# Kernel tuning notes

Measured on AMD Instinct MI355X. Metric: run time of the kernel, lower is better.

The kernel has to match this reference:

```python
import jax, jax.numpy as jnp
import numpy as np

N_HEADS = 8

def setup_inputs() -> dict:
    key = jax.random.key(0)
    ks = jax.random.split(key, 5)
    C = 256
    x = jax.random.normal(ks[0], (4, C, 48, 48), dtype=jnp.float32)
    w_qkv = jax.random.normal(ks[1], (3 * C, C), dtype=jnp.float32) * (C ** -0.5)
    b_qkv = jax.random.normal(ks[2], (3 * C,), dtype=jnp.float32) * 0.02
    w_proj = jax.random.normal(ks[3], (C, C), dtype=jnp.float32) * (C ** -0.5)
    b_proj = jax.random.normal(ks[4], (C,), dtype=jnp.float32) * 0.02
    return {"x": x, "w_qkv": w_qkv, "b_qkv": b_qkv, "w_proj": w_proj, "b_proj": b_proj}


def reference(x, w_qkv, b_qkv, w_proj, b_proj):
    B, C, H, W = x.shape
    h = N_HEADS
    dh = C // h
    N = H * W
    # flatten spatial dims to tokens: [B, N, C]
    xf = x.reshape(B, C, N).transpose(0, 2, 1)
    # fused qkv projection (torch Linear: y = x @ W.T + b)
    qkv = xf @ w_qkv.T + b_qkv                      # [B, N, 3C]
    qkv = qkv.reshape(B, N, 3, h, dh).transpose(2, 0, 3, 1, 4)  # [3, B, h, N, dh]
    q, k, v = qkv[0], qkv[1], qkv[2]
    scale = dh ** -0.5
    attn = jax.nn.softmax(jnp.einsum('bhnd,bhmd->bhnm', q, k) * scale, axis=-1)
    out = jnp.einsum('bhnm,bhmd->bhnd', attn, v)    # [B, h, N, dh]
    out = out.transpose(0, 2, 1, 3).reshape(B, N, C)
    out = out @ w_proj.T + b_proj                   # [B, N, C]
    return out.transpose(0, 2, 1).reshape(B, C, H, W)
```

## Files before the change

### kernel.cpp

```cpp
#include <hip/hip_runtime.h>
#include <hip/hip_bf16.h>

#define B_    4
#define C_    256
#define NTOK  2304
#define NH    8
#define DH    32

typedef short bf16x8 __attribute__((ext_vector_type(8)));
typedef short bf16x4 __attribute__((ext_vector_type(4)));
typedef float f32x4  __attribute__((ext_vector_type(4)));

__device__ __forceinline__ short f2bf(float f) {
    __hip_bfloat16 h = __float2bfloat16(f);
    return *reinterpret_cast<short*>(&h);
}

__global__ __launch_bounds__(256) void prep_kernel(
    const float* __restrict__ x, const float* __restrict__ wq,
    const float* __restrict__ wp,
    short* __restrict__ xt, short* __restrict__ wqb, short* __restrict__ wpb)
{
    const int blk = blockIdx.x;
    const int t   = threadIdx.x;
    if (blk < 576) {
        const int b  = blk / 144;
        const int rem = blk % 144;
        const int n0 = (rem / 4) * 64;
        const int c0 = (rem % 4) * 64;
        __shared__ float tile[64][65];
        const float* xb = x + ((size_t)b * C_ + c0) * NTOK + n0;
        const int n = t & 63, cc = t >> 6;
        #pragma unroll
        for (int r = 0; r < 16; ++r)
            tile[cc + r * 4][n] = xb[(size_t)(cc + r * 4) * NTOK + n];
        __syncthreads();
        const int nr = t >> 2, cb = (t & 3) * 16;
        short* dst = xt + ((size_t)b * NTOK + n0 + nr) * C_ + c0 + cb;
        bf16x8 v0, v1;
        #pragma unroll
        for (int u = 0; u < 8; ++u) v0[u] = f2bf(tile[cb + u][nr]);
        #pragma unroll
        for (int u = 0; u < 8; ++u) v1[u] = f2bf(tile[cb + 8 + u][nr]);
        *(bf16x8*)dst = v0;
        *(bf16x8*)(dst + 8) = v1;
    } else {
        const int id = (blk - 576) * 256 + t;
        const int base = id * 16;
        #pragma unroll
        for (int u = 0; u < 4; ++u) {
            const int off = base + u * 4;
            float4 v; short* d;
            if (off < 196608) { v = *(const float4*)(wq + off); d = wqb + off; }
            else { v = *(const float4*)(wp + (off - 196608)); d = wpb + (off - 196608); }
            d[0] = f2bf(v.x); d[1] = f2bf(v.y); d[2] = f2bf(v.z); d[3] = f2bf(v.w);
        }
    }
}

__global__ __launch_bounds__(256) void qkv_mfma(
    const short* __restrict__ xt,
    const short* __restrict__ wqb,
    const float* __restrict__ bias,
    short* __restrict__ qb, short* __restrict__ kb, short* __restrict__ vt)
{
    const int wid  = blockIdx.x * 4 + (threadIdx.x >> 6);
    const int lane = threadIdx.x & 63;
    const int quad = lane >> 4, l16 = lane & 15;
    const int b   = wid / 432;
    const int rem = wid % 432;
    const int mt = rem / 12, nt = rem % 12;
    const int m0 = mt * 64, j0 = nt * 64;

    const short* abase = xt + ((size_t)b * NTOK + m0 + l16) * C_ + quad * 8;
    const short* bbase = wqb + (size_t)(j0 + l16) * C_ + quad * 8;

    f32x4 acc[4][4] = {};
    for (int k0 = 0; k0 < C_; k0 += 32) {
        bf16x8 af[4], bfr[4];
        #pragma unroll
        for (int i = 0; i < 4; ++i)
            af[i] = *(const bf16x8*)(abase + (size_t)i * 16 * C_ + k0);
        #pragma unroll
        for (int j = 0; j < 4; ++j)
            bfr[j] = *(const bf16x8*)(bbase + (size_t)j * 16 * C_ + k0);
        #pragma unroll
        for (int i = 0; i < 4; ++i)
            #pragma unroll
            for (int j = 0; j < 4; ++j)
                acc[i][j] = __builtin_amdgcn_mfma_f32_16x16x32_bf16(af[i], bfr[j], acc[i][j], 0, 0, 0);
    }

    const int three = j0 >> 8;
    const float scale = 0.17677669529663687f;
    #pragma unroll
    for (int j = 0; j < 4; ++j) {
        const int jg   = j0 + j * 16 + l16;
        const int head = (jg >> 5) & 7;
        const int d    = jg & 31;
        const float bv = bias[jg];
        const size_t bhbase = (size_t)(b * NH + head) * NTOK;
        #pragma unroll
        for (int i = 0; i < 4; ++i) {
            if (three == 2) {
                bf16x4 pv;
                #pragma unroll
                for (int r = 0; r < 4; ++r) pv[r] = f2bf(acc[i][j][r] + bv);
                *(bf16x4*)(vt + ((size_t)(b * NH + head) * DH + d) * NTOK
                              + m0 + i * 16 + quad * 4) = pv;
            } else {
                short* dst = (three == 0) ? qb : kb;
                const float sc = (three == 0) ? scale : 1.0f;
                #pragma unroll
                for (int r = 0; r < 4; ++r) {
                    const int n = m0 + i * 16 + quad * 4 + r;
                    dst[(bhbase + n) * DH + d] = f2bf((acc[i][j][r] + bv) * sc);
                }
            }
        }
    }
}

__global__ __launch_bounds__(256) void attn_kernel(
    const short* __restrict__ qg,
    const short* __restrict__ kg,
    const short* __restrict__ vg,
    short* __restrict__ ob)
{
    const int bh   = blockIdx.y;
    const int q0   = blockIdx.x * 64;
    const int t    = threadIdx.x;
    const int wave = t >> 6;
    const int lane = t & 63;
    const int quad = lane >> 4;
    const int l16  = lane & 15;

    __shared__ short Ks[64][40];
    __shared__ short Vt[32][72];
    __shared__ short Ps[4][16][68];

    const short* kbase = kg + (size_t)bh * NTOK * DH;
    const short* vbase = vg + (size_t)bh * DH * NTOK;

    const short* qptr = qg + ((size_t)bh * NTOK + q0 + wave * 16 + l16) * DH + quad * 8;
    const bf16x8 qf = *(const bf16x8*)qptr;

    f32x4 Oc0 = {0.f, 0.f, 0.f, 0.f};
    f32x4 Oc1 = {0.f, 0.f, 0.f, 0.f};
    float lpart[4] = {0.f, 0.f, 0.f, 0.f};

    for (int kt = 0; kt < NTOK; kt += 64) {
        {
            const int kr = t >> 2, ksg = t & 3;
            *(bf16x8*)&Ks[kr][ksg * 8] =
                *(const bf16x8*)(kbase + (size_t)(kt + kr) * DH + ksg * 8);
            const int vr = t >> 3, vsg = t & 7;
            *(bf16x8*)&Vt[vr][vsg * 8] =
                *(const bf16x8*)(vbase + (size_t)vr * NTOK + kt + vsg * 8);
        }
        __syncthreads();

        f32x4 S[4];
        #pragma unroll
        for (int jt = 0; jt < 4; ++jt) {
            const bf16x8 kf = *(const bf16x8*)&Ks[jt * 16 + l16][quad * 8];
            f32x4 z = {0.f, 0.f, 0.f, 0.f};
            S[jt] = __builtin_amdgcn_mfma_f32_16x16x32_bf16(qf, kf, z, 0, 0, 0);
        }

        #pragma unroll
        for (int jt = 0; jt < 4; ++jt) {
            #pragma unroll
            for (int r = 0; r < 4; ++r) {
                const float p = __expf(S[jt][r]);
                lpart[r] += p;
                Ps[wave][quad * 4 + r][jt * 16 + l16] = f2bf(p);
            }
        }

        #pragma unroll
        for (int jc = 0; jc < 2; ++jc) {
            const bf16x4 p0 = *(const bf16x4*)&Ps[wave][l16][jc * 32 + quad * 8];
            const bf16x4 p1 = *(const bf16x4*)&Ps[wave][l16][jc * 32 + quad * 8 + 4];
            bf16x8 af;
            af[0] = p0[0]; af[1] = p0[1]; af[2] = p0[2]; af[3] = p0[3];
            af[4] = p1[0]; af[5] = p1[1]; af[6] = p1[2]; af[7] = p1[3];
            const bf16x8 b0 = *(const bf16x8*)&Vt[l16][jc * 32 + quad * 8];
            const bf16x8 b1 = *(const bf16x8*)&Vt[16 + l16][jc * 32 + quad * 8];
            Oc0 = __builtin_amdgcn_mfma_f32_16x16x32_bf16(af, b0, Oc0, 0, 0, 0);
            Oc1 = __builtin_amdgcn_mfma_f32_16x16x32_bf16(af, b1, Oc1, 0, 0, 0);
        }
        __syncthreads();
    }

    #pragma unroll
    for (int off = 1; off < 16; off <<= 1) {
        #pragma unroll
        for (int r = 0; r < 4; ++r)
            lpart[r] += __shfl_xor(lpart[r], off, 64);
    }
    short* obase = ob + ((size_t)bh * NTOK + q0 + wave * 16 + quad * 4) * DH + l16;
    #pragma unroll
    for (int r = 0; r < 4; ++r) {
        const float inv = 1.f / lpart[r];
        obase[(size_t)r * DH]      = f2bf(Oc0[r] * inv);
        obase[(size_t)r * DH + 16] = f2bf(Oc1[r] * inv);
    }
}

__global__ __launch_bounds__(256) void proj_mfma(
    const short* __restrict__ ab,
    const short* __restrict__ wpb,
    const float* __restrict__ bias,
    float* __restrict__ out)
{
    const int wid  = blockIdx.x * 4 + (threadIdx.x >> 6);
    const int lane = threadIdx.x & 63;
    const int quad = lane >> 4, l16 = lane & 15;
    const int b   = wid / 144;
    const int rem = wid % 144;
    const int mt = rem / 4, nt = rem % 4;
    const int m0 = mt * 64, c0 = nt * 64;

    const short* bbase = wpb + (size_t)(c0 + l16) * C_ + quad * 8;

    f32x4 acc[4][4] = {};
    for (int kt = 0; kt < 8; ++kt) {
        const short* abase = ab + ((size_t)(b * NH + kt) * NTOK + m0 + l16) * DH + quad * 8;
        bf16x8 af[4], bfr[4];
        #pragma unroll
        for (int i = 0; i < 4; ++i)
            af[i] = *(const bf16x8*)(abase + (size_t)i * 16 * DH);
        #pragma unroll
        for (int j = 0; j < 4; ++j)
            bfr[j] = *(const bf16x8*)(bbase + (size_t)j * 16 * C_ + kt * 32);
        #pragma unroll
        for (int i = 0; i < 4; ++i)
            #pragma unroll
            for (int j = 0; j < 4; ++j)
                acc[i][j] = __builtin_amdgcn_mfma_f32_16x16x32_bf16(af[i], bfr[j], acc[i][j], 0, 0, 0);
    }

    #pragma unroll
    for (int j = 0; j < 4; ++j) {
        const int c    = c0 + j * 16 + l16;
        const float bv = bias[c];
        #pragma unroll
        for (int i = 0; i < 4; ++i) {
            float4 st = {acc[i][j][0] + bv, acc[i][j][1] + bv,
                         acc[i][j][2] + bv, acc[i][j][3] + bv};
            *(float4*)(out + ((size_t)b * C_ + c) * NTOK + m0 + i * 16 + quad * 4) = st;
        }
    }
}

extern "C" void kernel_launch(void* const* d_in, const int* in_sizes, int n_in,
                              void* d_out, int out_size, void* d_ws, size_t ws_size,
                              hipStream_t stream) {
    const float* x      = (const float*)d_in[0];
    const float* w_qkv  = (const float*)d_in[1];
    const float* b_qkv  = (const float*)d_in[2];
    const float* w_proj = (const float*)d_in[3];
    const float* b_proj = (const float*)d_in[4];
    float* out = (float*)d_out;

    const size_t SZ = (size_t)B_ * NH * NTOK * DH;
    short* xt  = (short*)d_ws;
    short* wqb = xt + SZ;
    short* wpb = wqb + 196608;
    short* qb  = wpb + 65536;
    short* kb  = qb + SZ;
    short* vt  = kb + SZ;
    short* abf = vt + SZ;

    prep_kernel<<<640, 256, 0, stream>>>(x, w_qkv, w_proj, xt, wqb, wpb);
    qkv_mfma<<<432, 256, 0, stream>>>(xt, wqb, b_qkv, qb, kb, vt);
    attn_kernel<<<dim3(36, 32), 256, 0, stream>>>(qb, kb, vt, abf);
    proj_mfma<<<144, 256, 0, stream>>>(abf, wpb, b_proj, out);
}
```

Measured before the change: 167.1 us.

## Halve GEMM tiles, stage epilogues through LDS, widen attention key tile, use exp2

The QKV and projection GEMMs now use 32-row tiles per wave and launch twice as many blocks. Their epilogues are staged through per-wave shared memory so that global stores become coalesced 16-byte vectors instead of scattered 2-byte or 4-byte writes. The attention loop processes 128 keys per iteration, which halves the number of barriers, and it computes exp2 with the log2(e) factor folded into the Q scale. A manual round-to-nearest-even bf16 conversion replaces the library call. The costs are more LDS use per block and fewer MFMA operations per loaded fragment in the GEMMs.

```diff
diff --git a/kernel.cpp b/kernel.cpp
--- a/kernel.cpp
+++ b/kernel.cpp
@@ -11,9 +11,20 @@
 typedef short bf16x4 __attribute__((ext_vector_type(4)));
 typedef float f32x4  __attribute__((ext_vector_type(4)));
 
-__device__ __forceinline__ short f2bf(float f) {
-    __hip_bfloat16 h = __float2bfloat16(f);
-    return *reinterpret_cast<short*>(&h);
+__device__ __forceinline__ short rne_bf16(float f) {
+    union { float f; unsigned u; } v; v.f = f;
+    const unsigned r = v.u + 0x7fffu + ((v.u >> 16) & 1u);
+    return (short)(r >> 16);
+}
+__device__ __forceinline__ unsigned pack2_bf16(float a, float b) {
+    return (unsigned)(unsigned short)rne_bf16(a) | ((unsigned)(unsigned short)rne_bf16(b) << 16);
+}
+__device__ __forceinline__ float fast_exp2(float x) {
+#if __has_builtin(__builtin_amdgcn_exp2f)
+    return __builtin_amdgcn_exp2f(x);
+#else
+    return exp2f(x);
+#endif
 }
 
 __global__ __launch_bounds__(256) void prep_kernel(
@@ -39,9 +50,9 @@
         short* dst = xt + ((size_t)b * NTOK + n0 + nr) * C_ + c0 + cb;
         bf16x8 v0, v1;
         #pragma unroll
-        for (int u = 0; u < 8; ++u) v0[u] = f2bf(tile[cb + u][nr]);
-        #pragma unroll
-        for (int u = 0; u < 8; ++u) v1[u] = f2bf(tile[cb + 8 + u][nr]);
+        for (int u = 0; u < 8; ++u) v0[u] = rne_bf16(tile[cb + u][nr]);
+        #pragma unroll
+        for (int u = 0; u < 8; ++u) v1[u] = rne_bf16(tile[cb + 8 + u][nr]);
         *(bf16x8*)dst = v0;
         *(bf16x8*)(dst + 8) = v1;
     } else {
@@ -53,7 +64,8 @@
             float4 v; short* d;
             if (off < 196608) { v = *(const float4*)(wq + off); d = wqb + off; }
             else { v = *(const float4*)(wp + (off - 196608)); d = wpb + (off - 196608); }
-            d[0] = f2bf(v.x); d[1] = f2bf(v.y); d[2] = f2bf(v.z); d[3] = f2bf(v.w);
+            d[0] = rne_bf16(v.x); d[1] = rne_bf16(v.y);
+            d[2] = rne_bf16(v.z); d[3] = rne_bf16(v.w);
         }
     }
 }
@@ -64,59 +76,79 @@
     const float* __restrict__ bias,
     short* __restrict__ qb, short* __restrict__ kb, short* __restrict__ vt)
 {
-    const int wid  = blockIdx.x * 4 + (threadIdx.x >> 6);
+    __shared__ short Es[4][2560];
+    const int wave = threadIdx.x >> 6;
     const int lane = threadIdx.x & 63;
     const int quad = lane >> 4, l16 = lane & 15;
-    const int b   = wid / 432;
-    const int rem = wid % 432;
+    const int wid  = blockIdx.x * 4 + wave;
+    const int b    = wid / 864;
+    const int rem  = wid % 864;
     const int mt = rem / 12, nt = rem % 12;
-    const int m0 = mt * 64, j0 = nt * 64;
+    const int m0 = mt * 32, j0 = nt * 64;
 
     const short* abase = xt + ((size_t)b * NTOK + m0 + l16) * C_ + quad * 8;
     const short* bbase = wqb + (size_t)(j0 + l16) * C_ + quad * 8;
 
-    f32x4 acc[4][4] = {};
+    f32x4 acc[2][4] = {};
     for (int k0 = 0; k0 < C_; k0 += 32) {
-        bf16x8 af[4], bfr[4];
-        #pragma unroll
-        for (int i = 0; i < 4; ++i)
+        bf16x8 af[2], bfr[4];
+        #pragma unroll
+        for (int i = 0; i < 2; ++i)
             af[i] = *(const bf16x8*)(abase + (size_t)i * 16 * C_ + k0);
         #pragma unroll
         for (int j = 0; j < 4; ++j)
             bfr[j] = *(const bf16x8*)(bbase + (size_t)j * 16 * C_ + k0);
         #pragma unroll
-        for (int i = 0; i < 4; ++i)
+        for (int i = 0; i < 2; ++i)
             #pragma unroll
             for (int j = 0; j < 4; ++j)
                 acc[i][j] = __builtin_amdgcn_mfma_f32_16x16x32_bf16(af[i], bfr[j], acc[i][j], 0, 0, 0);
     }
 
+    short* Ew = Es[wave];
     const int three = j0 >> 8;
-    const float scale = 0.17677669529663687f;
-    #pragma unroll
-    for (int j = 0; j < 4; ++j) {
-        const int jg   = j0 + j * 16 + l16;
-        const int head = (jg >> 5) & 7;
-        const int d    = jg & 31;
-        const float bv = bias[jg];
-        const size_t bhbase = (size_t)(b * NH + head) * NTOK;
-        #pragma unroll
-        for (int i = 0; i < 4; ++i) {
-            if (three == 2) {
-                bf16x4 pv;
-                #pragma unroll
-                for (int r = 0; r < 4; ++r) pv[r] = f2bf(acc[i][j][r] + bv);
-                *(bf16x4*)(vt + ((size_t)(b * NH + head) * DH + d) * NTOK
-                              + m0 + i * 16 + quad * 4) = pv;
-            } else {
-                short* dst = (three == 0) ? qb : kb;
-                const float sc = (three == 0) ? scale : 1.0f;
+    if (three < 2) {
+        const float sc = (three == 0) ? 0.25503486f : 1.0f;
+        #pragma unroll
+        for (int j = 0; j < 4; ++j) {
+            const float bv = bias[j0 + j * 16 + l16];
+            #pragma unroll
+            for (int i = 0; i < 2; ++i)
                 #pragma unroll
                 for (int r = 0; r < 4; ++r) {
-                    const int n = m0 + i * 16 + quad * 4 + r;
-                    dst[(bhbase + n) * DH + d] = f2bf((acc[i][j][r] + bv) * sc);
+                    const int n_l = i * 16 + quad * 4 + r;
+                    Ew[n_l * 72 + j * 16 + l16] = rne_bf16((acc[i][j][r] + bv) * sc);
                 }
+        }
+        const int n_l = lane & 31, hh = lane >> 5;
+        const int head = ((j0 + hh * 32) >> 5) & 7;
+        short* dst = ((three == 0) ? qb : kb)
+                   + ((size_t)(b * NH + head) * NTOK + m0 + n_l) * DH;
+        #pragma unroll
+        for (int s = 0; s < 4; ++s)
+            *(bf16x8*)(dst + s * 8) = *(const bf16x8*)&Ew[n_l * 72 + hh * 32 + s * 8];
+    } else {
+        #pragma unroll
+        for (int j = 0; j < 4; ++j) {
+            const float bv = bias[j0 + j * 16 + l16];
+            const int j_l = j * 16 + l16;
+            #pragma unroll
+            for (int i = 0; i < 2; ++i) {
+                const int nb = i * 16 + quad * 4;
+                *(unsigned*)&Ew[j_l * 40 + nb] =
+                    pack2_bf16(acc[i][j][0] + bv, acc[i][j][1] + bv);
+                *(unsigned*)&Ew[j_l * 40 + nb + 2] =
+                    pack2_bf16(acc[i][j][2] + bv, acc[i][j][3] + bv);
             }
+        }
+        #pragma unroll
+        for (int p = 0; p < 4; ++p) {
+            const int j_r = p * 16 + (lane >> 2);
+            const int seg = (lane & 3) * 8;
+            const int head = ((j0 + j_r) >> 5) & 7;
+            const int d    = j_r & 31;
+            *(bf16x8*)(vt + ((size_t)(b * NH + head) * DH + d) * NTOK + m0 + seg) =
+                *(const bf16x8*)&Ew[j_r * 40 + seg];
         }
     }
 }
@@ -135,9 +167,9 @@
     const int quad = lane >> 4;
     const int l16  = lane & 15;
 
-    __shared__ short Ks[64][40];
-    __shared__ short Vt[32][72];
-    __shared__ short Ps[4][16][68];
+    __shared__ short Ks[128][40];
+    __shared__ short Vt[32][168];
+    __shared__ short Ps[4][16][140];
 
     const short* kbase = kg + (size_t)bh * NTOK * DH;
     const short* vbase = vg + (size_t)bh * DH * NTOK;
@@ -149,37 +181,39 @@
     f32x4 Oc1 = {0.f, 0.f, 0.f, 0.f};
     float lpart[4] = {0.f, 0.f, 0.f, 0.f};
 
-    for (int kt = 0; kt < NTOK; kt += 64) {
-        {
-            const int kr = t >> 2, ksg = t & 3;
-            *(bf16x8*)&Ks[kr][ksg * 8] =
-                *(const bf16x8*)(kbase + (size_t)(kt + kr) * DH + ksg * 8);
-            const int vr = t >> 3, vsg = t & 7;
-            *(bf16x8*)&Vt[vr][vsg * 8] =
-                *(const bf16x8*)(vbase + (size_t)vr * NTOK + kt + vsg * 8);
+    for (int kt = 0; kt < NTOK; kt += 128) {
+        #pragma unroll
+        for (int u = 0; u < 2; ++u) {
+            const int chunk = u * 256 + t;
+            const int krow = chunk >> 2, kseg = chunk & 3;
+            *(bf16x8*)&Ks[krow][kseg * 8] =
+                *(const bf16x8*)(kbase + (size_t)(kt + krow) * DH + kseg * 8);
+            const int vr = chunk >> 4, vs = chunk & 15;
+            *(bf16x8*)&Vt[vr][vs * 8] =
+                *(const bf16x8*)(vbase + (size_t)vr * NTOK + kt + vs * 8);
         }
         __syncthreads();
 
-        f32x4 S[4];
-        #pragma unroll
-        for (int jt = 0; jt < 4; ++jt) {
+        f32x4 S[8];
+        #pragma unroll
+        for (int jt = 0; jt < 8; ++jt) {
             const bf16x8 kf = *(const bf16x8*)&Ks[jt * 16 + l16][quad * 8];
             f32x4 z = {0.f, 0.f, 0.f, 0.f};
             S[jt] = __builtin_amdgcn_mfma_f32_16x16x32_bf16(qf, kf, z, 0, 0, 0);
         }
 
         #pragma unroll
-        for (int jt = 0; jt < 4; ++jt) {
+        for (int jt = 0; jt < 8; ++jt) {
             #pragma unroll
             for (int r = 0; r < 4; ++r) {
-                const float p = __expf(S[jt][r]);
+                const float p = fast_exp2(S[jt][r]);
                 lpart[r] += p;
-                Ps[wave][quad * 4 + r][jt * 16 + l16] = f2bf(p);
+                Ps[wave][quad * 4 + r][jt * 16 + l16] = rne_bf16(p);
             }
         }
 
         #pragma unroll
-        for (int jc = 0; jc < 2; ++jc) {
+        for (int jc = 0; jc < 4; ++jc) {
             const bf16x4 p0 = *(const bf16x4*)&Ps[wave][l16][jc * 32 + quad * 8];
             const bf16x4 p1 = *(const bf16x4*)&Ps[wave][l16][jc * 32 + quad * 8 + 4];
             bf16x8 af;
@@ -203,8 +237,8 @@
     #pragma unroll
     for (int r = 0; r < 4; ++r) {
         const float inv = 1.f / lpart[r];
-        obase[(size_t)r * DH]      = f2bf(Oc0[r] * inv);
-        obase[(size_t)r * DH + 16] = f2bf(Oc1[r] * inv);
+        obase[(size_t)r * DH]      = rne_bf16(Oc0[r] * inv);
+        obase[(size_t)r * DH + 16] = rne_bf16(Oc1[r] * inv);
     }
 }
 
@@ -214,43 +248,53 @@
     const float* __restrict__ bias,
     float* __restrict__ out)
 {
-    const int wid  = blockIdx.x * 4 + (threadIdx.x >> 6);
+    __shared__ float Ep[4][2304];
+    const int wave = threadIdx.x >> 6;
     const int lane = threadIdx.x & 63;
     const int quad = lane >> 4, l16 = lane & 15;
-    const int b   = wid / 144;
-    const int rem = wid % 144;
-    const int mt = rem / 4, nt = rem % 4;
-    const int m0 = mt * 64, c0 = nt * 64;
+    const int wid  = blockIdx.x * 4 + wave;
+    const int b    = wid / 288;
+    const int rem  = wid % 288;
+    const int mt = rem / 4, ct = rem % 4;
+    const int m0 = mt * 32, c0 = ct * 64;
 
     const short* bbase = wpb + (size_t)(c0 + l16) * C_ + quad * 8;
 
-    f32x4 acc[4][4] = {};
+    f32x4 acc[2][4] = {};
     for (int kt = 0; kt < 8; ++kt) {
         const short* abase = ab + ((size_t)(b * NH + kt) * NTOK + m0 + l16) * DH + quad * 8;
-        bf16x8 af[4], bfr[4];
-        #pragma unroll
-        for (int i = 0; i < 4; ++i)
+        bf16x8 af[2], bfr[4];
+        #pragma unroll
+        for (int i = 0; i < 2; ++i)
             af[i] = *(const bf16x8*)(abase + (size_t)i * 16 * DH);
         #pragma unroll
         for (int j = 0; j < 4; ++j)
             bfr[j] = *(const bf16x8*)(bbase + (size_t)j * 16 * C_ + kt * 32);
         #pragma unroll
-        for (int i = 0; i < 4; ++i)
+        for (int i = 0; i < 2; ++i)
             #pragma unroll
             for (int j = 0; j < 4; ++j)
                 acc[i][j] = __builtin_amdgcn_mfma_f32_16x16x32_bf16(af[i], bfr[j], acc[i][j], 0, 0, 0);
     }
 
+    float* Ew = Ep[wave];
     #pragma unroll
     for (int j = 0; j < 4; ++j) {
-        const int c    = c0 + j * 16 + l16;
-        const float bv = bias[c];
-        #pragma unroll
-        for (int i = 0; i < 4; ++i) {
-            float4 st = {acc[i][j][0] + bv, acc[i][j][1] + bv,
-                         acc[i][j][2] + bv, acc[i][j][3] + bv};
-            *(float4*)(out + ((size_t)b * C_ + c) * NTOK + m0 + i * 16 + quad * 4) = st;
-        }
+        const int j_l = j * 16 + l16;
+        const float bv = bias[c0 + j_l];
+        #pragma unroll
+        for (int i = 0; i < 2; ++i) {
+            f32x4 st = {acc[i][j][0] + bv, acc[i][j][1] + bv,
+                        acc[i][j][2] + bv, acc[i][j][3] + bv};
+            *(f32x4*)&Ew[j_l * 36 + i * 16 + quad * 4] = st;
+        }
+    }
+    #pragma unroll
+    for (int p = 0; p < 8; ++p) {
+        const int c_r = p * 8 + (lane >> 3);
+        const int seg = (lane & 7) * 4;
+        *(float4*)(out + ((size_t)b * C_ + c0 + c_r) * NTOK + m0 + seg) =
+            *(const float4*)&Ew[c_r * 36 + seg];
     }
 }
 
@@ -274,7 +318,7 @@
     short* abf = vt + SZ;
 
     prep_kernel<<<640, 256, 0, stream>>>(x, w_qkv, w_proj, xt, wqb, wpb);
-    qkv_mfma<<<432, 256, 0, stream>>>(xt, wqb, b_qkv, qb, kb, vt);
+    qkv_mfma<<<864, 256, 0, stream>>>(xt, wqb, b_qkv, qb, kb, vt);
     attn_kernel<<<dim3(36, 32), 256, 0, stream>>>(qb, kb, vt, abf);
-    proj_mfma<<<144, 256, 0, stream>>>(abf, wpb, b_proj, out);
-}
+    proj_mfma<<<288, 256, 0, stream>>>(abf, wpb, b_proj, out);
+}
```

Measured after the change: 193.5 us. +15.8%, slower.
